# Performance work log

Hardware: AMD Instinct MI355X
Metric: run time of the kernel (lower is better)

The kernel has to match this reference:

```python
import jax, jax.numpy as jnp
import numpy as np

B, I, H = 16384, 512, 512
HH = H // 2


def _lrelu(v):
    return jnp.where(v > 0, v, 0.01 * v)


def setup_inputs() -> dict:
    key = jax.random.key(0)
    ks = jax.random.split(key, 20)
    s = 1.0 / np.sqrt(H)
    rn = lambda k, shp, sc: (jax.random.normal(k, shp, jnp.float32) * sc)
    return {
        "x": rn(ks[0], (B, I), 1.0),
        "h0": rn(ks[1], (1, B, H), 1.0),
        "c0": rn(ks[2], (1, B, H), 1.0),
        "cum": jax.random.uniform(ks[3], (B, 1), jnp.float32),
        # LSTM params (torch gate order i, f, g, o)
        "W_ih": rn(ks[4], (4 * H, I), s),
        "W_hh": rn(ks[5], (4 * H, H), s),
        "b_ih": rn(ks[6], (4 * H,), s),
        "b_hh": rn(ks[7], (4 * H,), s),
        # skip gate MLP
        "W_sp": rn(ks[8], (HH, H), s),
        "b_sp": rn(ks[9], (HH,), s),
        "W_sc": rn(ks[10], (HH, H), s),
        "b_sc": rn(ks[11], (HH,), s),
        "W_so": rn(ks[12], (1, HH), s),
        "b_so": rn(ks[13], (1,), s),
        # threshold gate MLP
        "W_tp": rn(ks[14], (HH, H), s),
        "b_tp": rn(ks[15], (HH,), s),
        "W_to": rn(ks[16], (1, HH), s),
        "b_to": rn(ks[17], (1,), s),
    }


def reference(x, h0, c0, cum, W_ih, W_hh, b_ih, b_hh,
              W_sp, b_sp, W_sc, b_sc, W_so, b_so,
              W_tp, b_tp, W_to, b_to):
    # single-step, single-layer LSTM
    gates = x @ W_ih.T + b_ih + h0[0] @ W_hh.T + b_hh  # [B, 4H]
    i_g, f_g, g_g, o_g = jnp.split(gates, 4, axis=-1)
    i_g = jax.nn.sigmoid(i_g)
    f_g = jax.nn.sigmoid(f_g)
    g_g = jnp.tanh(g_g)
    o_g = jax.nn.sigmoid(o_g)
    c1l = f_g * c0[0] + i_g * g_g          # [B, H]
    h1l = o_g * jnp.tanh(c1l)              # [B, H]
    h1, c1 = h1l[None], c1l[None]          # [1, B, H]

    # skip gate: delta prob from c0[-1], c1[-1]
    sg = _lrelu(c0[-1] @ W_sp.T + b_sp + c1[-1] @ W_sc.T + b_sc)  # [B, H/2]
    update_prob_delta = jax.nn.sigmoid(sg @ W_so.T + b_so)        # [B, 1]

    # threshold gate from c0[-1]
    tg = _lrelu(c0[-1] @ W_tp.T + b_tp)                           # [B, H/2]
    update_threshold = jax.nn.sigmoid(tg @ W_to.T + b_to)         # [B, 1]

    update_prob = cum + jnp.minimum(update_prob_delta, 1.0 - cum)  # [B, 1]
    # straight-through round: fwd hard threshold, bwd identity to prob
    hard = (update_prob > update_threshold).astype(jnp.float32)
    update_gate = update_prob + jax.lax.stop_gradient(hard - update_prob)

    new_h = update_gate * h1 + (1.0 - update_gate) * h0  # [1, B, H]
    new_c = update_gate * c1 + (1.0 - update_gate) * c0  # [1, B, H]
    update_cum = (1.0 - update_gate) * update_prob        # [B, 1]
    return (new_h, new_c, update_cum, update_prob_delta, update_prob)
```

## Files before the change

### kernel.cpp

```cpp
#include <hip/hip_runtime.h>
#include <math.h>

#define BB 16384
#define HH 512

typedef short short8 __attribute__((ext_vector_type(8)));
typedef float f32x4 __attribute__((ext_vector_type(4)));
typedef unsigned short ushort_t;

__device__ __forceinline__ float sigm(float v){ return 1.0f/(1.0f+expf(-v)); }

__device__ __forceinline__ unsigned short f2bf(float f){
    unsigned int u = __float_as_uint(f);
    u = u + 0x7FFFu + ((u>>16)&1u);
    return (unsigned short)(u>>16);
}
__device__ __forceinline__ float bf2f(unsigned short h){
    return __uint_as_float(((unsigned int)h)<<16);
}
__device__ __forceinline__ void gll16(const void* g, void* l){
    __builtin_amdgcn_global_load_lds((const __attribute__((address_space(1))) void*)g,
                                     (__attribute__((address_space(3))) void*)l, 16, 0, 0);
}
__device__ __forceinline__ void split_store(float v, ushort_t* ph, ushort_t* pl, int j){
    unsigned short h = f2bf(v);
    unsigned short l = f2bf(v - bf2f(h));
    ph[j] = h; pl[j] = l;
}

__global__ void k_prep_all(
    const float* __restrict__ x, const float* __restrict__ h0, const float* __restrict__ c0,
    const float* __restrict__ W_ih, const float* __restrict__ W_hh,
    const float* __restrict__ b_ih, const float* __restrict__ b_hh,
    const float* __restrict__ W_sp, const float* __restrict__ W_sc, const float* __restrict__ W_tp,
    const float* __restrict__ b_sp, const float* __restrict__ b_sc, const float* __restrict__ b_tp,
    ushort_t* __restrict__ A1h, ushort_t* __restrict__ A1l,
    ushort_t* __restrict__ A2h, ushort_t* __restrict__ A2l,
    ushort_t* __restrict__ B1h, ushort_t* __restrict__ B1l,
    ushort_t* __restrict__ B2h, ushort_t* __restrict__ B2l,
    float* __restrict__ bgp, float* __restrict__ bs2)
{
    int bid = blockIdx.x;
    if (bid < 8192) {
        int u = bid*256 + threadIdx.x;
        int r  = u & 255;
        int c  = (u >> 8) & 3;
        int kt = (u >> 10) & 31;
        int tm = u >> 15;
        int row = tm*256 + r;
        int k0 = kt*32 + c*8;
        const float* src = (k0 < 512) ? (x + (size_t)row*512 + k0)
                                      : (h0 + (size_t)row*512 + (k0-512));
        float4 v0 = *(const float4*)(src);
        float4 v1 = *(const float4*)(src+4);
        float vv[8] = {v0.x,v0.y,v0.z,v0.w,v1.x,v1.y,v1.z,v1.w};
        size_t off = (size_t)u * 8;
#pragma unroll
        for (int j=0;j<8;++j) split_store(vv[j], A1h+off, A1l+off, j);
    } else if (bid < 12288) {
        int u = (bid-8192)*256 + threadIdx.x;
        int r  = u & 127;
        int c  = (u >> 7) & 3;
        int tk = (u >> 9) & 15;
        int tm = u >> 13;
        int row = tm*128 + r;
        int k0 = tk*32 + c*8;
        const float* src = c0 + (size_t)row*512 + k0;
        float4 v0 = *(const float4*)(src);
        float4 v1 = *(const float4*)(src+4);
        float vv[8] = {v0.x,v0.y,v0.z,v0.w,v1.x,v1.y,v1.z,v1.w};
        size_t off = ((size_t)tm*32 + tk)*4096 + (size_t)(c*128 + r)*8;
#pragma unroll
        for (int j=0;j<8;++j) split_store(vv[j], A2h+off, A2l+off, j);
    } else if (bid < 13312) {
        int u = (bid-12288)*256 + threadIdx.x;
        int r  = u & 255;
        int c  = (u >> 8) & 3;
        int kt = (u >> 10) & 31;
        int tn = u >> 15;
        int g = (r>>4)&3;
        int h = tn*64 + (r>>6)*16 + (r&15);
        int wrow = g*512 + h;
        int k0 = kt*32 + c*8;
        const float* src = (k0 < 512) ? (W_ih + (size_t)wrow*512 + k0)
                                      : (W_hh + (size_t)wrow*512 + (k0-512));
        float4 v0 = *(const float4*)(src);
        float4 v1 = *(const float4*)(src+4);
        float vv[8] = {v0.x,v0.y,v0.z,v0.w,v1.x,v1.y,v1.z,v1.w};
        size_t off = (size_t)u * 8;
#pragma unroll
        for (int j=0;j<8;++j) split_store(vv[j], B1h+off, B1l+off, j);
        if (kt == 0 && c == 0) bgp[tn*256 + r] = b_ih[wrow] + b_hh[wrow];
    } else {
        int u = (bid-13312)*256 + threadIdx.x;
        int r  = u & 127;
        int c  = (u >> 7) & 3;
        int tk = (u >> 9) & 31;
        int tn = u >> 14;
        int n = tn*128 + r;
        int k0 = tk*32 + c*8;
        float vv[8];
        if (n < 256) {
            const float* src = (k0 < 512) ? (W_sp + (size_t)n*512 + k0)
                                          : (W_sc + (size_t)n*512 + (k0-512));
            float4 v0 = *(const float4*)(src);
            float4 v1 = *(const float4*)(src+4);
            vv[0]=v0.x; vv[1]=v0.y; vv[2]=v0.z; vv[3]=v0.w;
            vv[4]=v1.x; vv[5]=v1.y; vv[6]=v1.z; vv[7]=v1.w;
        } else if (k0 < 512) {
            const float* src = W_tp + (size_t)(n-256)*512 + k0;
            float4 v0 = *(const float4*)(src);
            float4 v1 = *(const float4*)(src+4);
            vv[0]=v0.x; vv[1]=v0.y; vv[2]=v0.z; vv[3]=v0.w;
            vv[4]=v1.x; vv[5]=v1.y; vv[6]=v1.z; vv[7]=v1.w;
        } else {
#pragma unroll
            for (int j=0;j<8;++j) vv[j] = 0.0f;
        }
        size_t off = (size_t)u * 8;
#pragma unroll
        for (int j=0;j<8;++j) split_store(vv[j], B2h+off, B2l+off, j);
        if (tk == 0 && c == 0) bs2[n] = (n < 256) ? (b_sp[n] + b_sc[n]) : b_tp[n-256];
    }
}

#define GSTEP(T, CA, CB, NA, NB, DO_READS, DO_STAGE, VMASM)                          \
  {                                                                                  \
    if (DO_READS) {                                                                  \
        const ushort_t* bufA1 = &lds[((T)+1) & 3][0];                                \
        const ushort_t* bufB1 = &lds[((T)+1) & 3][8192];                             \
        _Pragma("unroll") for (int f = 0; f < 8; ++f)                                \
            NA[f] = *(const short8*)&bufA1[aoff[f]];                                 \
        _Pragma("unroll") for (int f = 0; f < 4; ++f)                                \
            NB[f] = *(const short8*)&bufB1[boff[f]];                                 \
    }                                                                                \
    if (DO_STAGE) {                                                                  \
        const int uu = (T) + 3;                                                      \
        const ushort_t* As_ = ((uu >> 5) == 1) ? Al : Ah;                            \
        const ushort_t* Bs_ = ((uu >> 5) == 2) ? Bl : Bh;                            \
        size_t ga = ((size_t)tm*32 + (uu & 31))*8192 + (size_t)tid*8;                \
        size_t gb = ((size_t)tn*32 + (uu & 31))*8192 + (size_t)tid*8;                \
        ushort_t* dA = &lds[uu & 3][0];                                              \
        ushort_t* dB = &lds[uu & 3][8192];                                           \
        gll16(As_ + ga,        dA + tid*8);                                          \
        gll16(As_ + ga + 4096, dA + 4096 + tid*8);                                   \
        gll16(Bs_ + gb,        dB + tid*8);                                          \
        gll16(Bs_ + gb + 4096, dB + 4096 + tid*8);                                   \
    }                                                                                \
    __builtin_amdgcn_sched_barrier(0);                                               \
    __builtin_amdgcn_s_setprio(1);                                                   \
    _Pragma("unroll") for (int fm = 0; fm < 8; ++fm)                                 \
        _Pragma("unroll") for (int fn = 0; fn < 4; ++fn)                             \
            acc[fm][fn] = __builtin_amdgcn_mfma_f32_16x16x32_bf16(CA[fm], CB[fn], acc[fm][fn], 0,0,0); \
    __builtin_amdgcn_s_setprio(0);                                                   \
    asm volatile("s_waitcnt lgkmcnt(0)" ::: "memory");                               \
    __builtin_amdgcn_sched_barrier(0);                                               \
    VMASM;                                                                           \
    asm volatile("s_barrier" ::: "memory");                                          \
  }

__global__ __launch_bounds__(512, 2) void k_gemm_gates(
    const ushort_t* __restrict__ Ah, const ushort_t* __restrict__ Al,
    const ushort_t* __restrict__ Bh, const ushort_t* __restrict__ Bl,
    const float* __restrict__ bgp, const float* __restrict__ c0,
    float* __restrict__ outH, float* __restrict__ outC,
    ushort_t* __restrict__ A2h, ushort_t* __restrict__ A2l)
{
    __shared__ __align__(16) ushort_t lds[4][16384];
    const int tid  = threadIdx.x;
    const int lane = tid & 63;
    const int wid  = tid >> 6;
    const int wr   = wid >> 2;
    const int wc   = wid & 3;
    const int l15  = lane & 15;
    const int lq   = lane >> 4;
    const int bid  = (int)blockIdx.x;
    const int v    = (bid & 7)*64 + (bid >> 3);
    const int tm   = v >> 3;
    const int tn   = v & 7;

    f32x4 acc[8][4];
#pragma unroll
    for (int fn = 0; fn < 4; ++fn) {
        float bv = bgp[tn*256 + wc*64 + fn*16 + l15];
#pragma unroll
        for (int fm = 0; fm < 8; ++fm) {
            acc[fm][fn][0]=bv; acc[fm][fn][1]=bv; acc[fm][fn][2]=bv; acc[fm][fn][3]=bv;
        }
    }

    int aoff[8], boff[4];
#pragma unroll
    for (int f = 0; f < 8; ++f) aoff[f] = (lq*256 + wr*128 + f*16 + l15) * 8;
#pragma unroll
    for (int f = 0; f < 4; ++f) boff[f] = (lq*256 + wc*64 + f*16 + l15) * 8;

    short8 a0[8], b0[4], a1[8], b1[4];

#pragma unroll
    for (int u0 = 0; u0 < 3; ++u0) {
        size_t ga = ((size_t)tm*32 + u0)*8192 + (size_t)tid*8;
        size_t gb = ((size_t)tn*32 + u0)*8192 + (size_t)tid*8;
        gll16(Ah + ga,        &lds[u0][0]     + tid*8);
        gll16(Ah + ga + 4096, &lds[u0][4096]  + tid*8);
        gll16(Bh + gb,        &lds[u0][8192]  + tid*8);
        gll16(Bh + gb + 4096, &lds[u0][12288] + tid*8);
    }
    asm volatile("s_waitcnt vmcnt(4)" ::: "memory");
    asm volatile("s_barrier" ::: "memory");
#pragma unroll
    for (int f = 0; f < 8; ++f) a0[f] = *(const short8*)&lds[0][aoff[f]];
#pragma unroll
    for (int f = 0; f < 4; ++f) b0[f] = *(const short8*)&lds[0][8192 + boff[f]];
    asm volatile("s_waitcnt lgkmcnt(0)" ::: "memory");
    __builtin_amdgcn_sched_barrier(0);

    for (int t = 0; t < 92; t += 2) {
        GSTEP(t,   a0, b0, a1, b1, 1, 1, asm volatile("s_waitcnt vmcnt(4)" ::: "memory"));
        GSTEP(t+1, a1, b1, a0, b0, 1, 1, asm volatile("s_waitcnt vmcnt(4)" ::: "memory"));
    }
    GSTEP(92, a0, b0, a1, b1, 1, 1, asm volatile("s_waitcnt vmcnt(4)" ::: "memory"));
    GSTEP(93, a1, b1, a0, b0, 1, 0, asm volatile("s_waitcnt vmcnt(0)" ::: "memory"));
    GSTEP(94, a0, b0, a1, b1, 1, 0, ((void)0));
    GSTEP(95, a1, b1, a0, b0, 0, 0, ((void)0));

    const int h = tn*64 + wc*16 + l15;
#pragma unroll
    for (int fm = 0; fm < 8; ++fm) {
        int row0 = tm*256 + wr*128 + fm*16 + lq*4;
#pragma unroll
        for (int r = 0; r < 4; ++r) {
            int row = row0 + r;
            size_t idx = (size_t)row*512 + h;
            float ig = sigm(acc[fm][0][r]);
            float fg = sigm(acc[fm][1][r]);
            float gg = tanhf(acc[fm][2][r]);
            float og = sigm(acc[fm][3][r]);
            float c1 = fg*c0[idx] + ig*gg;
            float h1 = og*tanhf(c1);
            outC[idx] = c1;
            outH[idx] = h1;
            unsigned short ch = f2bf(c1);
            unsigned short cl = f2bf(c1 - bf2f(ch));
            size_t a2 = ((size_t)(row>>7)*32 + 16 + (h>>5))*4096
                      + (size_t)((((h>>3)&3))*128 + (row&127))*8 + (h&7);
            A2h[a2] = ch;
            A2l[a2] = cl;
        }
    }
}

#define SSTEP(T, CA, CB, NA, NB, DO_READS, DO_STAGE, VMASM)                          \
  {                                                                                  \
    if (DO_READS) {                                                                  \
        const ushort_t* bufA1 = &lds2[((T)+1) & 3][0];                               \
        const ushort_t* bufB1 = &lds2[((T)+1) & 3][4096];                            \
        _Pragma("unroll") for (int f = 0; f < 4; ++f)                                \
            NA[f] = *(const short8*)&bufA1[aoff[f]];                                 \
        _Pragma("unroll") for (int f = 0; f < 4; ++f)                                \
            NB[f] = *(const short8*)&bufB1[boff[f]];                                 \
    }                                                                                \
    if (DO_STAGE) {                                                                  \
        const int uu = (T) + 3;                                                      \
        const ushort_t* As_ = ((uu >> 5) == 1) ? Al : Ah;                            \
        const ushort_t* Bs_ = ((uu >> 5) == 2) ? Bl : Bh;                            \
        size_t ga = ((size_t)tm*32 + (uu & 31))*4096 + (size_t)tid*8;                \
        size_t gb = ((size_t)tn*32 + (uu & 31))*4096 + (size_t)tid*8;                \
        ushort_t* dA = &lds2[uu & 3][0];                                             \
        ushort_t* dB = &lds2[uu & 3][4096];                                          \
        gll16(As_ + ga,        dA + tid*8);                                          \
        gll16(As_ + ga + 2048, dA + 2048 + tid*8);                                   \
        gll16(Bs_ + gb,        dB + tid*8);                                          \
        gll16(Bs_ + gb + 2048, dB + 2048 + tid*8);                                   \
    }                                                                                \
    __builtin_amdgcn_sched_barrier(0);                                               \
    __builtin_amdgcn_s_setprio(1);                                                   \
    _Pragma("unroll") for (int fm = 0; fm < 4; ++fm)                                 \
        _Pragma("unroll") for (int fn = 0; fn < 4; ++fn)                             \
            acc[fm][fn] = __builtin_amdgcn_mfma_f32_16x16x32_bf16(CA[fm], CB[fn], acc[fm][fn], 0,0,0); \
    __builtin_amdgcn_s_setprio(0);                                                   \
    asm volatile("s_waitcnt lgkmcnt(0)" ::: "memory");                               \
    __builtin_amdgcn_sched_barrier(0);                                               \
    VMASM;                                                                           \
    asm volatile("s_barrier" ::: "memory");                                          \
  }

__global__ __launch_bounds__(256, 2) void k_gemm_sgtg(
    const ushort_t* __restrict__ Ah, const ushort_t* __restrict__ Al,
    const ushort_t* __restrict__ Bh, const ushort_t* __restrict__ Bl,
    const float* __restrict__ bs2,
    float* __restrict__ sgtg)
{
    __shared__ __align__(16) ushort_t lds2[4][8192];
    const int tid  = threadIdx.x;
    const int lane = tid & 63;
    const int wid  = tid >> 6;
    const int wr   = wid >> 1;
    const int wc   = wid & 1;
    const int l15  = lane & 15;
    const int lq   = lane >> 4;
    const int bid  = (int)blockIdx.x;
    const int v    = (bid & 7)*64 + (bid >> 3);
    const int tm   = v >> 2;
    const int tn   = v & 3;

    f32x4 acc[4][4];
#pragma unroll
    for (int fn = 0; fn < 4; ++fn) {
        float bv = bs2[tn*128 + wc*64 + fn*16 + l15];
#pragma unroll
        for (int fm = 0; fm < 4; ++fm) {
            acc[fm][fn][0]=bv; acc[fm][fn][1]=bv; acc[fm][fn][2]=bv; acc[fm][fn][3]=bv;
        }
    }

    int aoff[4], boff[4];
#pragma unroll
    for (int f = 0; f < 4; ++f) {
        aoff[f] = (lq*128 + wr*64 + f*16 + l15) * 8;
        boff[f] = (lq*128 + wc*64 + f*16 + l15) * 8;
    }

    short8 a0[4], b0[4], a1[4], b1[4];

#pragma unroll
    for (int u0 = 0; u0 < 3; ++u0) {
        size_t ga = ((size_t)tm*32 + u0)*4096 + (size_t)tid*8;
        size_t gb = ((size_t)tn*32 + u0)*4096 + (size_t)tid*8;
        gll16(Ah + ga,        &lds2[u0][0]    + tid*8);
        gll16(Ah + ga + 2048, &lds2[u0][2048] + tid*8);
        gll16(Bh + gb,        &lds2[u0][4096] + tid*8);
        gll16(Bh + gb + 2048, &lds2[u0][6144] + tid*8);
    }
    asm volatile("s_waitcnt vmcnt(4)" ::: "memory");
    asm volatile("s_barrier" ::: "memory");
#pragma unroll
    for (int f = 0; f < 4; ++f) a0[f] = *(const short8*)&lds2[0][aoff[f]];
#pragma unroll
    for (int f = 0; f < 4; ++f) b0[f] = *(const short8*)&lds2[0][4096 + boff[f]];
    asm volatile("s_waitcnt lgkmcnt(0)" ::: "memory");
    __builtin_amdgcn_sched_barrier(0);

    for (int t = 0; t < 92; t += 2) {
        SSTEP(t,   a0, b0, a1, b1, 1, 1, asm volatile("s_waitcnt vmcnt(4)" ::: "memory"));
        SSTEP(t+1, a1, b1, a0, b0, 1, 1, asm volatile("s_waitcnt vmcnt(4)" ::: "memory"));
    }
    SSTEP(92, a0, b0, a1, b1, 1, 1, asm volatile("s_waitcnt vmcnt(4)" ::: "memory"));
    SSTEP(93, a1, b1, a0, b0, 1, 0, asm volatile("s_waitcnt vmcnt(0)" ::: "memory"));
    SSTEP(94, a0, b0, a1, b1, 1, 0, ((void)0));
    SSTEP(95, a1, b1, a0, b0, 0, 0, ((void)0));

#pragma unroll
    for (int fm = 0; fm < 4; ++fm) {
        int row0 = tm*128 + wr*64 + fm*16 + lq*4;
#pragma unroll
        for (int fn = 0; fn < 4; ++fn) {
            int n = tn*128 + wc*64 + fn*16 + l15;
#pragma unroll
            for (int r = 0; r < 4; ++r) {
                int row = row0 + r;
                float vv = acc[fm][fn][r];
                vv = vv > 0.f ? vv : 0.01f*vv;
                sgtg[(size_t)row*512 + n] = vv;
            }
        }
    }
}

__global__ __launch_bounds__(256) void k_final(
    const float* __restrict__ sgtg,
    const float* __restrict__ h0, const float* __restrict__ c0,
    const float* __restrict__ cum,
    const float* __restrict__ W_so, const float* __restrict__ b_so,
    const float* __restrict__ W_to, const float* __restrict__ b_to,
    float* __restrict__ outH, float* __restrict__ outC,
    float* __restrict__ outCum, float* __restrict__ outDelta, float* __restrict__ outProb)
{
    int w = threadIdx.x >> 6;
    int lane = threadIdx.x & 63;
    int b = blockIdx.x * 4 + w;
    const float* row = sgtg + (size_t)b * 512;
    float so = 0.f, to = 0.f;
#pragma unroll
    for (int u = 0; u < 4; ++u) {
        int c = lane + 64 * u;
        so = fmaf(row[c], W_so[c], so);
        to = fmaf(row[256 + c], W_to[c], to);
    }
#pragma unroll
    for (int off = 32; off; off >>= 1) {
        so += __shfl_down(so, off);
        to += __shfl_down(to, off);
    }
    so = __shfl(so, 0);
    to = __shfl(to, 0);
    float delta = sigm(so + b_so[0]);
    float thr   = sigm(to + b_to[0]);
    float cu = cum[b];
    float prob = cu + fminf(delta, 1.0f - cu);
    float hard = (prob > thr) ? 1.0f : 0.0f;
    if (lane == 0) {
        outDelta[b] = delta;
        outProb[b]  = prob;
        outCum[b]   = (1.0f - hard) * prob;
    }
    if (hard == 0.0f) {
#pragma unroll
        for (int u = 0; u < 8; ++u) {
            size_t idx = (size_t)b * 512 + lane + 64 * u;
            outH[idx] = h0[idx];
            outC[idx] = c0[idx];
        }
    }
}

extern "C" void kernel_launch(void* const* d_in, const int* in_sizes, int n_in,
                              void* d_out, int out_size, void* d_ws, size_t ws_size,
                              hipStream_t stream)
{
    const float* x    = (const float*)d_in[0];
    const float* h0   = (const float*)d_in[1];
    const float* c0   = (const float*)d_in[2];
    const float* cum  = (const float*)d_in[3];
    const float* W_ih = (const float*)d_in[4];
    const float* W_hh = (const float*)d_in[5];
    const float* b_ih = (const float*)d_in[6];
    const float* b_hh = (const float*)d_in[7];
    const float* W_sp = (const float*)d_in[8];
    const float* b_sp = (const float*)d_in[9];
    const float* W_sc = (const float*)d_in[10];
    const float* b_sc = (const float*)d_in[11];
    const float* W_so = (const float*)d_in[12];
    const float* b_so = (const float*)d_in[13];
    const float* W_tp = (const float*)d_in[14];
    const float* b_tp = (const float*)d_in[15];
    const float* W_to = (const float*)d_in[16];
    const float* b_to = (const float*)d_in[17];

    float* out      = (float*)d_out;
    float* outH     = out;
    float* outC     = out + (size_t)BB * HH;
    float* outCum   = out + (size_t)2 * BB * HH;
    float* outDelta = outCum + BB;
    float* outProb  = outDelta + BB;

    char* w = (char*)d_ws;
    ushort_t* A1h = (ushort_t*)(w);
    ushort_t* A1l = (ushort_t*)(w + 33554432ull);
    ushort_t* A2h = (ushort_t*)(w + 67108864ull);
    ushort_t* A2l = (ushort_t*)(w + 100663296ull);
    ushort_t* B1h = (ushort_t*)(w + 134217728ull);
    ushort_t* B1l = (ushort_t*)(w + 138412032ull);
    ushort_t* B2h = (ushort_t*)(w + 142606336ull);
    ushort_t* B2l = (ushort_t*)(w + 143654912ull);
    float*    bgp = (float*)(w + 144703488ull);
    float*    bs2 = (float*)(w + 144711680ull);
    float*    sgtg = (float*)A1h;

    k_prep_all<<<13568, 256, 0, stream>>>(x, h0, c0, W_ih, W_hh, b_ih, b_hh,
                                          W_sp, W_sc, W_tp, b_sp, b_sc, b_tp,
                                          A1h, A1l, A2h, A2l, B1h, B1l, B2h, B2l,
                                          bgp, bs2);
    k_gemm_gates<<<512, 512, 0, stream>>>(A1h, A1l, B1h, B1l, bgp, c0,
                                          outH, outC, A2h, A2l);
    k_gemm_sgtg<<<512, 256, 0, stream>>>(A2h, A2l, B2h, B2l, bs2, sgtg);
    k_final<<<4096, 256, 0, stream>>>(sgtg, h0, c0, cum, W_so, b_so, W_to, b_to,
                                      outH, outC, outCum, outDelta, outProb);
}
```

Measured before the change: 340.0 us.

## Restructure gates GEMM into 4-phase ping-pong with K=64 tiles and relaid operands

The gates GEMM main loop moves from 96 K=32 steps over a 4-deep LDS ring to 48 K=64 steps over a 2-buffer LDS layout. Each step is split into four quadrant phases, and each phase stages one half-tile for the next step while MFMAs run on the current one. The prep kernel's A1/B1 packing and the bias layout are reordered to match the new quadrant and fragment layout. The aim is fewer barriers per FLOP and better overlap of global-to-LDS loads with MFMA work. In exchange it adds more s_barrier calls per step and a fragile hand-written wait and staging schedule.

```diff
diff --git a/kernel.cpp b/kernel.cpp
--- a/kernel.cpp
+++ b/kernel.cpp
@@ -43,12 +43,14 @@
     int bid = blockIdx.x;
     if (bid < 8192) {
         int u = bid*256 + threadIdx.x;
-        int r  = u & 255;
-        int c  = (u >> 8) & 3;
-        int kt = (u >> 10) & 31;
-        int tm = u >> 15;
-        int row = tm*256 + r;
-        int k0 = kt*32 + c*8;
+        int rr   = u & 127;
+        int c    = (u >> 7) & 7;
+        int half = (u >> 10) & 1;
+        int kt   = (u >> 11) & 15;
+        int tm   = u >> 15;
+        int wr = rr >> 6, q2 = (rr >> 4) & 3, l15 = rr & 15;
+        int row = tm*256 + wr*128 + (half*4 + q2)*16 + l15;
+        int k0  = kt*64 + c*8;
         const float* src = (k0 < 512) ? (x + (size_t)row*512 + k0)
                                       : (h0 + (size_t)row*512 + (k0-512));
         float4 v0 = *(const float4*)(src);
@@ -74,14 +76,16 @@
         for (int j=0;j<8;++j) split_store(vv[j], A2h+off, A2l+off, j);
     } else if (bid < 13312) {
         int u = (bid-12288)*256 + threadIdx.x;
-        int r  = u & 255;
-        int c  = (u >> 8) & 3;
-        int kt = (u >> 10) & 31;
-        int tn = u >> 15;
-        int g = (r>>4)&3;
-        int h = tn*64 + (r>>6)*16 + (r&15);
+        int cc   = u & 127;
+        int c    = (u >> 7) & 7;
+        int half = (u >> 10) & 1;
+        int kt   = (u >> 11) & 15;
+        int tn   = u >> 15;
+        int wcg = cc >> 5, fn1 = (cc >> 4) & 1, h16 = cc & 15;
+        int g = half*2 + fn1;
+        int h = tn*64 + wcg*16 + h16;
         int wrow = g*512 + h;
-        int k0 = kt*32 + c*8;
+        int k0 = kt*64 + c*8;
         const float* src = (k0 < 512) ? (W_ih + (size_t)wrow*512 + k0)
                                       : (W_hh + (size_t)wrow*512 + (k0-512));
         float4 v0 = *(const float4*)(src);
@@ -90,7 +94,7 @@
         size_t off = (size_t)u * 8;
 #pragma unroll
         for (int j=0;j<8;++j) split_store(vv[j], B1h+off, B1l+off, j);
-        if (kt == 0 && c == 0) bgp[tn*256 + r] = b_ih[wrow] + b_hh[wrow];
+        if (kt == 0 && c == 0) bgp[tn*256 + g*64 + wcg*16 + h16] = b_ih[wrow] + b_hh[wrow];
     } else {
         int u = (bid-13312)*256 + threadIdx.x;
         int r  = u & 127;
@@ -124,40 +128,23 @@
     }
 }
 
-#define GSTEP(T, CA, CB, NA, NB, DO_READS, DO_STAGE, VMASM)                          \
-  {                                                                                  \
-    if (DO_READS) {                                                                  \
-        const ushort_t* bufA1 = &lds[((T)+1) & 3][0];                                \
-        const ushort_t* bufB1 = &lds[((T)+1) & 3][8192];                             \
-        _Pragma("unroll") for (int f = 0; f < 8; ++f)                                \
-            NA[f] = *(const short8*)&bufA1[aoff[f]];                                 \
-        _Pragma("unroll") for (int f = 0; f < 4; ++f)                                \
-            NB[f] = *(const short8*)&bufB1[boff[f]];                                 \
-    }                                                                                \
-    if (DO_STAGE) {                                                                  \
-        const int uu = (T) + 3;                                                      \
-        const ushort_t* As_ = ((uu >> 5) == 1) ? Al : Ah;                            \
-        const ushort_t* Bs_ = ((uu >> 5) == 2) ? Bl : Bh;                            \
-        size_t ga = ((size_t)tm*32 + (uu & 31))*8192 + (size_t)tid*8;                \
-        size_t gb = ((size_t)tn*32 + (uu & 31))*8192 + (size_t)tid*8;                \
-        ushort_t* dA = &lds[uu & 3][0];                                              \
-        ushort_t* dB = &lds[uu & 3][8192];                                           \
-        gll16(As_ + ga,        dA + tid*8);                                          \
-        gll16(As_ + ga + 4096, dA + 4096 + tid*8);                                   \
-        gll16(Bs_ + gb,        dB + tid*8);                                          \
-        gll16(Bs_ + gb + 4096, dB + 4096 + tid*8);                                   \
-    }                                                                                \
-    __builtin_amdgcn_sched_barrier(0);                                               \
-    __builtin_amdgcn_s_setprio(1);                                                   \
-    _Pragma("unroll") for (int fm = 0; fm < 8; ++fm)                                 \
-        _Pragma("unroll") for (int fn = 0; fn < 4; ++fn)                             \
-            acc[fm][fn] = __builtin_amdgcn_mfma_f32_16x16x32_bf16(CA[fm], CB[fn], acc[fm][fn], 0,0,0); \
-    __builtin_amdgcn_s_setprio(0);                                                   \
+#define QUAD(AF, BF, R0, C0)                                                         \
+    _Pragma("unroll") for (int i2 = 0; i2 < 4; ++i2)                                 \
+    _Pragma("unroll") for (int j2 = 0; j2 < 2; ++j2) {                               \
+        acc[(R0)+i2][(C0)+j2] = __builtin_amdgcn_mfma_f32_16x16x32_bf16(             \
+            AF[i2][0], BF[j2][0], acc[(R0)+i2][(C0)+j2], 0,0,0);                     \
+        acc[(R0)+i2][(C0)+j2] = __builtin_amdgcn_mfma_f32_16x16x32_bf16(             \
+            AF[i2][1], BF[j2][1], acc[(R0)+i2][(C0)+j2], 0,0,0);                     \
+    }
+
+#define STAGEH(SRC, GBASE, LDST)                                                     \
+    gll16((SRC) + (GBASE) + (size_t)tid*8, (LDST) + tid*8);                          \
+    gll16((SRC) + (GBASE) + 4096 + (size_t)tid*8, (LDST) + 4096 + tid*8);
+
+#define PH_SYNC                                                                      \
+    asm volatile("s_barrier" ::: "memory");                                          \
     asm volatile("s_waitcnt lgkmcnt(0)" ::: "memory");                               \
-    __builtin_amdgcn_sched_barrier(0);                                               \
-    VMASM;                                                                           \
-    asm volatile("s_barrier" ::: "memory");                                          \
-  }
+    __builtin_amdgcn_sched_barrier(0);
 
 __global__ __launch_bounds__(512, 2) void k_gemm_gates(
     const ushort_t* __restrict__ Ah, const ushort_t* __restrict__ Al,
@@ -166,7 +153,7 @@
     float* __restrict__ outH, float* __restrict__ outC,
     ushort_t* __restrict__ A2h, ushort_t* __restrict__ A2l)
 {
-    __shared__ __align__(16) ushort_t lds[4][16384];
+    __shared__ __align__(16) ushort_t lds[2][32768];
     const int tid  = threadIdx.x;
     const int lane = tid & 63;
     const int wid  = tid >> 6;
@@ -182,47 +169,98 @@
     f32x4 acc[8][4];
 #pragma unroll
     for (int fn = 0; fn < 4; ++fn) {
-        float bv = bgp[tn*256 + wc*64 + fn*16 + l15];
+        float bv = bgp[tn*256 + fn*64 + wc*16 + l15];
 #pragma unroll
         for (int fm = 0; fm < 8; ++fm) {
             acc[fm][fn][0]=bv; acc[fm][fn][1]=bv; acc[fm][fn][2]=bv; acc[fm][fn][3]=bv;
         }
     }
 
-    int aoff[8], boff[4];
-#pragma unroll
-    for (int f = 0; f < 8; ++f) aoff[f] = (lq*256 + wr*128 + f*16 + l15) * 8;
-#pragma unroll
-    for (int f = 0; f < 4; ++f) boff[f] = (lq*256 + wc*64 + f*16 + l15) * 8;
-
-    short8 a0[8], b0[4], a1[8], b1[4];
-
-#pragma unroll
-    for (int u0 = 0; u0 < 3; ++u0) {
-        size_t ga = ((size_t)tm*32 + u0)*8192 + (size_t)tid*8;
-        size_t gb = ((size_t)tn*32 + u0)*8192 + (size_t)tid*8;
-        gll16(Ah + ga,        &lds[u0][0]     + tid*8);
-        gll16(Ah + ga + 4096, &lds[u0][4096]  + tid*8);
-        gll16(Bh + gb,        &lds[u0][8192]  + tid*8);
-        gll16(Bh + gb + 4096, &lds[u0][12288] + tid*8);
-    }
-    asm volatile("s_waitcnt vmcnt(4)" ::: "memory");
+    int aro[8][2], bro[4][2];
+#pragma unroll
+    for (int fm = 0; fm < 8; ++fm)
+#pragma unroll
+        for (int kk = 0; kk < 2; ++kk)
+            aro[fm][kk] = (fm>>2)*8192 + (kk*4+lq)*1024 + (wr*64 + (fm&3)*16 + l15)*8;
+#pragma unroll
+    for (int fn = 0; fn < 4; ++fn)
+#pragma unroll
+        for (int kk = 0; kk < 2; ++kk)
+            bro[fn][kk] = 16384 + (fn>>1)*8192 + (kk*4+lq)*1024 + (wc*32 + (fn&1)*16 + l15)*8;
+
+    short8 a0[4][2], a1[4][2], b0[2][2], b1[2][2];
+
+    {
+        STAGEH(Ah, (size_t)((tm*16 + 0)*2 + 0)*8192, &lds[0][0]);
+        STAGEH(Bh, (size_t)((tn*16 + 0)*2 + 0)*8192, &lds[0][16384]);
+        STAGEH(Ah, (size_t)((tm*16 + 0)*2 + 1)*8192, &lds[0][8192]);
+        STAGEH(Bh, (size_t)((tn*16 + 0)*2 + 1)*8192, &lds[0][24576]);
+        STAGEH(Ah, (size_t)((tm*16 + 1)*2 + 0)*8192, &lds[1][0]);
+    }
+    asm volatile("s_waitcnt vmcnt(2)" ::: "memory");
     asm volatile("s_barrier" ::: "memory");
-#pragma unroll
-    for (int f = 0; f < 8; ++f) a0[f] = *(const short8*)&lds[0][aoff[f]];
-#pragma unroll
-    for (int f = 0; f < 4; ++f) b0[f] = *(const short8*)&lds[0][8192 + boff[f]];
-    asm volatile("s_waitcnt lgkmcnt(0)" ::: "memory");
-    __builtin_amdgcn_sched_barrier(0);
-
-    for (int t = 0; t < 92; t += 2) {
-        GSTEP(t,   a0, b0, a1, b1, 1, 1, asm volatile("s_waitcnt vmcnt(4)" ::: "memory"));
-        GSTEP(t+1, a1, b1, a0, b0, 1, 1, asm volatile("s_waitcnt vmcnt(4)" ::: "memory"));
-    }
-    GSTEP(92, a0, b0, a1, b1, 1, 1, asm volatile("s_waitcnt vmcnt(4)" ::: "memory"));
-    GSTEP(93, a1, b1, a0, b0, 1, 0, asm volatile("s_waitcnt vmcnt(0)" ::: "memory"));
-    GSTEP(94, a0, b0, a1, b1, 1, 0, ((void)0));
-    GSTEP(95, a1, b1, a0, b0, 0, 0, ((void)0));
+
+    for (int t = 0; t < 48; ++t) {
+        const int u1 = t + 1, u2 = t + 2;
+        const ushort_t* sA1 = ((u1 >> 4) == 1) ? Al : Ah;
+        const ushort_t* sB1 = ((u1 >> 4) == 2) ? Bl : Bh;
+        const ushort_t* sA2 = ((u2 >> 4) == 1) ? Al : Ah;
+        const int ki1 = u1 & 15, ki2 = u2 & 15;
+        const int st1 = (t <= 46), st4 = (t <= 45);
+        ushort_t* bufc = &lds[t & 1][0];
+        ushort_t* bufn = &lds[(t+1) & 1][0];
+
+#pragma unroll
+        for (int i2 = 0; i2 < 4; ++i2) {
+            a0[i2][0] = *(const short8*)&bufc[aro[i2][0]];
+            a0[i2][1] = *(const short8*)&bufc[aro[i2][1]];
+        }
+#pragma unroll
+        for (int j2 = 0; j2 < 2; ++j2) {
+            b0[j2][0] = *(const short8*)&bufc[bro[j2][0]];
+            b0[j2][1] = *(const short8*)&bufc[bro[j2][1]];
+        }
+        if (st1) { STAGEH(sB1, (size_t)((tn*16 + ki1)*2 + 0)*8192, bufn + 16384); }
+        PH_SYNC;
+        __builtin_amdgcn_s_setprio(1);
+        QUAD(a0, b0, 0, 0);
+        __builtin_amdgcn_s_setprio(0);
+        asm volatile("s_barrier" ::: "memory");
+
+#pragma unroll
+        for (int i2 = 0; i2 < 4; ++i2) {
+            a1[i2][0] = *(const short8*)&bufc[aro[4+i2][0]];
+            a1[i2][1] = *(const short8*)&bufc[aro[4+i2][1]];
+        }
+        if (st1) { STAGEH(sA1, (size_t)((tm*16 + ki1)*2 + 1)*8192, bufn + 8192); }
+        PH_SYNC;
+        __builtin_amdgcn_s_setprio(1);
+        QUAD(a1, b0, 4, 0);
+        __builtin_amdgcn_s_setprio(0);
+        asm volatile("s_barrier" ::: "memory");
+
+#pragma unroll
+        for (int j2 = 0; j2 < 2; ++j2) {
+            b1[j2][0] = *(const short8*)&bufc[bro[2+j2][0]];
+            b1[j2][1] = *(const short8*)&bufc[bro[2+j2][1]];
+        }
+        if (st1) { STAGEH(sB1, (size_t)((tn*16 + ki1)*2 + 1)*8192, bufn + 24576); }
+        PH_SYNC;
+        __builtin_amdgcn_s_setprio(1);
+        QUAD(a1, b1, 4, 2);
+        __builtin_amdgcn_s_setprio(0);
+        asm volatile("s_barrier" ::: "memory");
+
+        if (st4) { STAGEH(sA2, (size_t)((tm*16 + ki2)*2 + 0)*8192, bufc + 0); }
+        if (t >= 46) { asm volatile("s_waitcnt vmcnt(0)" ::: "memory"); }
+        else         { asm volatile("s_waitcnt vmcnt(2)" ::: "memory"); }
+        __builtin_amdgcn_sched_barrier(0);
+        asm volatile("s_barrier" ::: "memory");
+        __builtin_amdgcn_s_setprio(1);
+        QUAD(a0, b1, 0, 2);
+        __builtin_amdgcn_s_setprio(0);
+        asm volatile("s_barrier" ::: "memory");
+    }
 
     const int h = tn*64 + wc*16 + l15;
 #pragma unroll
```

New measurement: 339.8 us. About the same (-0.1%).
